# Performance work log

Measured on AMD Instinct MI355X. Metric: run time of the kernel, lower is better.

Reference implementation:

```python
import jax, jax.numpy as jnp
import numpy as np

B, L, T, LM, DFF, D, H = 8, 256, 2048, 4096, 1024, 84, 4
HD = D // H  # 21
NCLS = 265


def _ln(x, s, b):
    m = x.mean(-1, keepdims=True)
    v = ((x - m) ** 2).mean(-1, keepdims=True)
    return (x - m) * jax.lax.rsqrt(v + 1e-5) * s + b


def _fourier(xyz, gB):
    # PositionEmbeddingCoordsSine(d_pos=10, pos_type='fourier'): xyz @ B * 2pi -> [sin, cos]
    proj = (2.0 * jnp.pi) * jnp.einsum('bnc,cd->bnd', xyz, gB)  # [B,N,5]
    return jnp.concatenate([jnp.sin(proj), jnp.cos(proj)], axis=-1)  # [B,N,10]


def setup_inputs() -> dict:
    key = jax.random.key(0)
    ks = jax.random.split(key, 20)
    def nrm(k, shape, scale):
        return jax.random.normal(k, shape, jnp.float32) * scale
    coords = jax.random.uniform(ks[0], (B, L, 6), jnp.float32)
    cls = jax.random.randint(ks[1], (B, L), 0, NCLS).astype(jnp.float32)
    vision_features = jnp.concatenate([coords, cls[..., None]], axis=-1)  # [B,L,7]
    FIN = D * L + LM  # 25600
    inp = {
        'grd_tokens': nrm(ks[2], (T, LM), 1.0),
        'vision_features': vision_features,
        'token_batch_idx': jax.random.randint(ks[3], (T,), 0, B),
        'gauss_B': nrm(ks[4], (3, 5), 1.0),
        'class_emb': nrm(ks[5], (NCLS, 64), 0.02),
        'w_in': nrm(ks[6], (2, D, 3 * D), D ** -0.5),
        'b_in': jnp.zeros((2, 3 * D), jnp.float32),
        'w_out': nrm(ks[7], (2, D, D), D ** -0.5),
        'b_out': jnp.zeros((2, D), jnp.float32),
        'ln1_s': jnp.ones((2, D), jnp.float32), 'ln1_b': jnp.zeros((2, D), jnp.float32),
        'w_ff1': nrm(ks[8], (2, D, DFF), D ** -0.5), 'b_ff1': jnp.zeros((2, DFF), jnp.float32),
        'w_ff2': nrm(ks[9], (2, DFF, D), DFF ** -0.5), 'b_ff2': jnp.zeros((2, D), jnp.float32),
        'ln2_s': jnp.ones((2, D), jnp.float32), 'ln2_b': jnp.zeros((2, D), jnp.float32),
        'w0': nrm(ks[10], (FIN, DFF), FIN ** -0.5), 'b0': jnp.zeros((DFF,), jnp.float32),
        'w1': nrm(ks[11], (DFF, DFF), DFF ** -0.5), 'b1': jnp.zeros((DFF,), jnp.float32),
        'w2': nrm(ks[12], (DFF, DFF), DFF ** -0.5), 'b2': jnp.zeros((DFF,), jnp.float32),
        'w3': nrm(ks[13], (DFF, DFF), DFF ** -0.5), 'b3': jnp.zeros((DFF,), jnp.float32),
        'w4': nrm(ks[14], (DFF, 6), DFF ** -0.5), 'b4': jnp.zeros((6,), jnp.float32),
    }
    return inp


def reference(grd_tokens, vision_features, token_batch_idx, gauss_B, class_emb,
              w_in, b_in, w_out, b_out, ln1_s, ln1_b, w_ff1, b_ff1, w_ff2, b_ff2,
              ln2_s, ln2_b, w0, b0, w1, b1, w2, b2, w3, b3, w4, b4):
    pe_min = _fourier(vision_features[:, :, 0:3], gauss_B)  # [B,L,10]
    pe_max = _fourier(vision_features[:, :, 3:6], gauss_B)  # [B,L,10]
    cls = vision_features[:, :, -1].astype(jnp.int32)
    src = jnp.concatenate([pe_min, pe_max, class_emb[cls]], axis=-1)  # [B,L,84]
    pad = jnp.all(vision_features == 0, axis=-1)  # [B,L]
    neg = jnp.where(pad, -1e9, 0.0)[:, None, None, :]  # [B,1,1,L] key-padding bias
    # 2-layer post-norm transformer encoder (DETR-style, pos=None, dropout=0)
    for l in range(2):
        qkv = src @ w_in[l] + b_in[l]
        q, k, v = jnp.split(qkv, 3, axis=-1)
        q = q.reshape(B, L, H, HD)
        k = k.reshape(B, L, H, HD)
        v = v.reshape(B, L, H, HD)
        scores = jnp.einsum('blhd,bmhd->bhlm', q, k) / jnp.sqrt(jnp.float32(HD)) + neg
        attn = jax.nn.softmax(scores, axis=-1)
        o = jnp.einsum('bhlm,bmhd->blhd', attn, v).reshape(B, L, D)
        src = _ln(src + o @ w_out[l] + b_out[l], ln1_s[l], ln1_b[l])
        ff = jax.nn.relu(src @ w_ff1[l] + b_ff1[l]) @ w_ff2[l] + b_ff2[l]
        src = _ln(src + ff, ln2_s[l], ln2_b[l])
    vision_flat = src.reshape(B, L * D)  # flattened encoder output per sample [B, 21504]
    # batched version of the ragged python loop: gather per-token vision feat + concat lm feat
    feat = jnp.concatenate([vision_flat[token_batch_idx], grd_tokens], axis=-1)  # [T, 25600]
    h = jax.nn.relu(feat @ w0 + b0)
    h = jax.nn.relu(h @ w1 + b1)
    h = jax.nn.relu(h @ w2 + b2)
    h = jax.nn.relu(h @ w3 + b3)
    return h @ w4 + b4  # [T, 6]
```

## Files before the change

### kernel.cpp

```cpp
#include <hip/hip_runtime.h>
#include <hip/hip_bf16.h>

#define B_ 8
#define L_ 256
#define T_ 2048
#define LM_ 4096
#define DFF_ 1024
#define D_ 84
#define H_ 4
#define HD_ 21
#define BL_ (B_*L_)
#define VISF_ (L_*D_)
#define VKS 168
#define VCHUNK (VISF_/VKS)
#define AKS 8
#define AKEYS (L_/AKS)

typedef __attribute__((ext_vector_type(8))) short bf16x8;
typedef __attribute__((ext_vector_type(4))) float f32x4;

typedef const __attribute__((address_space(1))) int* gas_p;
typedef __attribute__((address_space(3))) int* las_p;
__device__ __forceinline__ void gld_lds16(const void* g, void* l) {
    __builtin_amdgcn_global_load_lds((gas_p)g, (las_p)l, 16, 0, 0);
}

__global__ void k_build_src(const float* __restrict__ vf, const float* __restrict__ gB,
                            const float* __restrict__ cemb, float* __restrict__ src,
                            float* __restrict__ neg)
{
    int row = blockIdx.x * blockDim.x + threadIdx.x;
    if (row >= BL_) return;
    float v[7];
    bool allz = true;
    #pragma unroll
    for (int c = 0; c < 7; ++c) { v[c] = vf[row*7 + c]; allz = allz && (v[c] == 0.0f); }
    neg[row] = allz ? -1e9f : 0.0f;
    float* s = src + (size_t)row * D_;
    const float TWO_PI = 6.28318530717958647692f;
    #pragma unroll
    for (int d = 0; d < 5; ++d) {
        float pmin = TWO_PI * (v[0]*gB[d] + v[1]*gB[5+d] + v[2]*gB[10+d]);
        float pmax = TWO_PI * (v[3]*gB[d] + v[4]*gB[5+d] + v[5]*gB[10+d]);
        s[d]      = sinf(pmin);  s[5+d]  = cosf(pmin);
        s[10+d]   = sinf(pmax);  s[15+d] = cosf(pmax);
    }
    int cls = (int)v[6];
    const float4* ce = reinterpret_cast<const float4*>(cemb + (size_t)cls*64);
    float4* so = reinterpret_cast<float4*>(s + 20);
    #pragma unroll
    for (int i = 0; i < 16; ++i) so[i] = ce[i];
}

__global__ __launch_bounds__(256) void k_qkv8(const float* __restrict__ src,
        const float* __restrict__ w_in, const float* __restrict__ b_in,
        float* __restrict__ qkv, int lay)
{
    __shared__ float s8[8][D_];
    int r0 = blockIdx.x * 8, tid = threadIdx.x;
    for (int idx = tid; idx < 8*D_; idx += 256) {
        int r = idx / D_, d = idx - r*D_;
        s8[r][d] = src[(size_t)(r0+r)*D_ + d];
    }
    __syncthreads();
    if (tid < 3*D_) {
        const float* w = w_in + (size_t)lay*D_*3*D_ + tid;
        float acc[8] = {};
        for (int d = 0; d < D_; ++d) {
            float wv = w[(size_t)d*3*D_];
            #pragma unroll
            for (int r = 0; r < 8; ++r) acc[r] = fmaf(s8[r][d], wv, acc[r]);
        }
        float bv = b_in[lay*3*D_ + tid];
        #pragma unroll
        for (int r = 0; r < 8; ++r) qkv[(size_t)(r0+r)*(3*D_) + tid] = acc[r] + bv;
    }
}

__global__ __launch_bounds__(256) void k_attn_part(const float* __restrict__ qkv,
        const float* __restrict__ neg, float* __restrict__ part)
{
    __shared__ float ks_[AKEYS*HD_], vs_[AKEYS*HD_], ns[AKEYS];
    int bh = blockIdx.x;
    int b = bh >> 2, h = bh & 3;
    int sp = blockIdx.y;
    int tid = threadIdx.x;
    int k0 = sp * AKEYS;
    for (int idx = tid; idx < AKEYS*HD_; idx += 256) {
        int l = idx / HD_, d = idx - l*HD_;
        size_t base = ((size_t)(b*L_ + k0 + l))*(3*D_) + h*HD_ + d;
        ks_[idx] = qkv[base + D_];
        vs_[idx] = qkv[base + 2*D_];
    }
    if (tid < AKEYS) ns[tid] = neg[b*L_ + k0 + tid];
    __syncthreads();
    float q[HD_];
    {
        size_t base = ((size_t)(b*L_ + tid))*(3*D_) + h*HD_;
        #pragma unroll
        for (int d = 0; d < HD_; ++d) q[d] = qkv[base + d];
    }
    const float scale = 0.21821789023599239f;
    float m_run = -INFINITY, l_run = 0.0f;
    float o[HD_];
    #pragma unroll
    for (int d = 0; d < HD_; ++d) o[d] = 0.0f;
    for (int m = 0; m < AKEYS; ++m) {
        const float* krow = &ks_[m*HD_];
        float sdot = 0.0f;
        #pragma unroll
        for (int d = 0; d < HD_; ++d) sdot = fmaf(q[d], krow[d], sdot);
        float sc = sdot * scale + ns[m];
        float nm = fmaxf(m_run, sc);
        float c = __expf(m_run - nm);
        float p = __expf(sc - nm);
        l_run = l_run * c + p;
        const float* vrow = &vs_[m*HD_];
        #pragma unroll
        for (int d = 0; d < HD_; ++d) o[d] = fmaf(p, vrow[d], o[d]*c);
        m_run = nm;
    }
    float* po = part + (((size_t)bh*AKS + sp)*L_ + tid)*24;
    #pragma unroll
    for (int d = 0; d < HD_; ++d) po[d] = o[d];
    po[21] = m_run;
    po[22] = l_run;
}

__global__ __launch_bounds__(128) void k_oproj_ln(const float* __restrict__ part,
        const float* __restrict__ w_out, const float* __restrict__ b_out,
        const float* __restrict__ ln_s, const float* __restrict__ ln_b,
        float* __restrict__ src, __hip_bfloat16* __restrict__ srcb, int lay)
{
    __shared__ float os[D_];
    __shared__ float r1[128], r2[128];
    int row = blockIdx.x, tid = threadIdx.x;
    int b = row >> 8, q = row & 255;
    if (tid < D_) {
        int h = tid / 21, d = tid - h*21;
        const float* pb = part + (((size_t)(b*H_ + h)*AKS)*L_ + q)*24;
        float m_tot = -INFINITY;
        #pragma unroll
        for (int sp = 0; sp < AKS; ++sp)
            m_tot = fmaxf(m_tot, pb[(size_t)sp*L_*24 + 21]);
        float l_tot = 0.0f, ov = 0.0f;
        #pragma unroll
        for (int sp = 0; sp < AKS; ++sp) {
            const float* pp = pb + (size_t)sp*L_*24;
            float e = __expf(pp[21] - m_tot);
            l_tot = fmaf(pp[22], e, l_tot);
            ov = fmaf(pp[d], e, ov);
        }
        os[tid] = ov / l_tot;
    }
    __syncthreads();
    float y = 0.0f;
    if (tid < D_) {
        const float* w = w_out + (size_t)lay*D_*D_ + tid;
        float acc = b_out[lay*D_ + tid];
        for (int d = 0; d < D_; ++d) acc = fmaf(os[d], w[(size_t)d*D_], acc);
        y = src[(size_t)row*D_ + tid] + acc;
    }
    r1[tid] = (tid < D_) ? y : 0.0f;
    r2[tid] = (tid < D_) ? y*y : 0.0f;
    __syncthreads();
    for (int s = 64; s > 0; s >>= 1) {
        if (tid < s) { r1[tid] += r1[tid+s]; r2[tid] += r2[tid+s]; }
        __syncthreads();
    }
    float mean = r1[0] * (1.0f/D_);
    float var  = r2[0] * (1.0f/D_) - mean*mean;
    float rstd = rsqrtf(var + 1e-5f);
    float out = 0.0f;
    if (tid < D_) {
        out = (y - mean)*rstd*ln_s[lay*D_+tid] + ln_b[lay*D_+tid];
        src[(size_t)row*D_ + tid] = out;
    }
    srcb[(size_t)row*128 + tid] = (tid < D_) ? __float2bfloat16(out)
                                             : __float2bfloat16(0.0f);
}

__global__ __launch_bounds__(256) void k_ff2_mfma(
        const __hip_bfloat16* __restrict__ hb,
        const __hip_bfloat16* __restrict__ wt,
        float* __restrict__ part)
{
    __shared__ __align__(16) __hip_bfloat16 sA[2][4096];
    __shared__ __align__(16) __hip_bfloat16 sB[2][6144];
    int tid = threadIdx.x;
    int bm = blockIdx.x * 64, sp = blockIdx.y;
    int wave = tid >> 6, lane = tid & 63;
    int wr = wave >> 1, wc = wave & 1;
    int l15 = lane & 15, l4 = lane >> 4;
    f32x4 acc[2][3] = {};

    const int a_m0 = tid & 63;
    const int b_i0 = tid,       b_kb0 = b_i0/96, b_n0 = b_i0%96;
    const int b_i1 = tid + 256, b_kb1 = b_i1/96, b_n1 = b_i1%96;
    const int b_i2 = tid + 512, b_kb2 = b_i2/96, b_n2 = b_i2%96;
    const __hip_bfloat16* Ap0 = hb + (size_t)(bm + a_m0)*1024 + sp*128 + (tid>>6)*8;
    const __hip_bfloat16* Ap1 = Ap0 + 32;
    const __hip_bfloat16* Bp0 = wt + (size_t)b_n0*1024 + sp*128 + b_kb0*8;
    const __hip_bfloat16* Bp1 = wt + (size_t)b_n1*1024 + sp*128 + b_kb1*8;
    const __hip_bfloat16* Bp2 = wt + (size_t)b_n2*1024 + sp*128 + b_kb2*8;

    gld_lds16(Ap0, (char*)&sA[0][0] + tid*16);
    gld_lds16(Ap1, (char*)&sA[0][0] + (tid+256)*16);
    gld_lds16(Bp0, (char*)&sB[0][0] + b_i0*16);
    gld_lds16(Bp1, (char*)&sB[0][0] + b_i1*16);
    gld_lds16(Bp2, (char*)&sB[0][0] + b_i2*16);
    #pragma unroll
    for (int t = 0; t < 2; ++t) {
        __syncthreads();
        if (t == 0) {
            gld_lds16(Ap0 + 64, (char*)&sA[1][0] + tid*16);
            gld_lds16(Ap1 + 64, (char*)&sA[1][0] + (tid+256)*16);
            gld_lds16(Bp0 + 64, (char*)&sB[1][0] + b_i0*16);
            gld_lds16(Bp1 + 64, (char*)&sB[1][0] + b_i1*16);
            gld_lds16(Bp2 + 64, (char*)&sB[1][0] + b_i2*16);
        }
        const __hip_bfloat16* sa = &sA[t][0];
        const __hip_bfloat16* sb = &sB[t][0];
        #pragma unroll
        for (int ks = 0; ks < 2; ++ks) {
            bf16x8 af[2], bfr[3];
            #pragma unroll
            for (int mi = 0; mi < 2; ++mi)
                af[mi] = *reinterpret_cast<const bf16x8*>(
                    &sa[(size_t)((ks*4 + l4)*64 + wr*32 + mi*16 + l15) * 8]);
            #pragma unroll
            for (int ni = 0; ni < 3; ++ni)
                bfr[ni] = *reinterpret_cast<const bf16x8*>(
                    &sb[(size_t)((ks*4 + l4)*96 + wc*48 + ni*16 + l15) * 8]);
            #pragma unroll
            for (int mi = 0; mi < 2; ++mi)
                #pragma unroll
                for (int ni = 0; ni < 3; ++ni)
                    acc[mi][ni] = __builtin_amdgcn_mfma_f32_16x16x32_bf16(
                        af[mi], bfr[ni], acc[mi][ni], 0, 0, 0);
        }
    }
    float* po = part + (size_t)sp*(2048*96);
    #pragma unroll
    for (int mi = 0; mi < 2; ++mi)
        #pragma unroll
        for (int reg = 0; reg < 4; ++reg) {
            int row = bm + wr*32 + mi*16 + l4*4 + reg;
            #pragma unroll
            for (int ni = 0; ni < 3; ++ni) {
                int col = wc*48 + ni*16 + l15;
                po[(size_t)row*96 + col] = acc[mi][ni][reg];
            }
        }
}

__global__ __launch_bounds__(128) void k_ff2ln_red(const float* __restrict__ part,
        const float* __restrict__ b_ff2, const float* __restrict__ ln_s,
        const float* __restrict__ ln_b, float* __restrict__ src, int lay)
{
    __shared__ float r1[128], r2[128];
    int row = blockIdx.x, tid = threadIdx.x;
    float y = 0.0f;
    if (tid < D_) {
        #pragma unroll
        for (int sp = 0; sp < 8; ++sp)
            y += part[(size_t)sp*(2048*96) + (size_t)row*96 + tid];
        y += b_ff2[lay*D_ + tid] + src[(size_t)row*D_ + tid];
    }
    r1[tid] = (tid < D_) ? y : 0.0f;
    r2[tid] = (tid < D_) ? y*y : 0.0f;
    __syncthreads();
    for (int s = 64; s > 0; s >>= 1) {
        if (tid < s) { r1[tid] += r1[tid+s]; r2[tid] += r2[tid+s]; }
        __syncthreads();
    }
    float mean = r1[0] * (1.0f/D_);
    float var  = r2[0] * (1.0f/D_) - mean*mean;
    float rstd = rsqrtf(var + 1e-5f);
    if (tid < D_)
        src[(size_t)row*D_ + tid] = (y - mean)*rstd*ln_s[lay*D_+tid] + ln_b[lay*D_+tid];
}

__global__ __launch_bounds__(256) void k_vis_gemm(const float* __restrict__ src,
        const float* __restrict__ w0, float* __restrict__ partials)
{
    __shared__ float vf[8][VCHUNK];
    __shared__ float red[8][256][4];
    int nt = blockIdx.x, sp = blockIdx.y, tid = threadIdx.x;
    int k0 = sp * VCHUNK;
    for (int idx = tid; idx < 8*VCHUNK; idx += 256) {
        int r = idx >> 7, c = idx & 127;
        vf[r][c] = src[(size_t)r*VISF_ + k0 + c];
    }
    __syncthreads();
    int ng = tid & 31;
    int kh = tid >> 5;
    const float* wp = w0 + (size_t)(k0 + kh*16)*DFF_ + nt*128 + ng*4;
    float acc[8][4] = {};
    #pragma unroll 4
    for (int kk = 0; kk < 16; ++kk) {
        float4 w = *reinterpret_cast<const float4*>(wp + (size_t)kk*DFF_);
        #pragma unroll
        for (int m = 0; m < 8; ++m) {
            float sv = vf[m][kh*16 + kk];
            acc[m][0] = fmaf(sv, w.x, acc[m][0]);
            acc[m][1] = fmaf(sv, w.y, acc[m][1]);
            acc[m][2] = fmaf(sv, w.z, acc[m][2]);
            acc[m][3] = fmaf(sv, w.w, acc[m][3]);
        }
    }
    #pragma unroll
    for (int m = 0; m < 8; ++m)
        *reinterpret_cast<float4*>(&red[m][tid][0]) =
            make_float4(acc[m][0], acc[m][1], acc[m][2], acc[m][3]);
    __syncthreads();
    int m2 = tid >> 5, ng2 = tid & 31;
    float4 s = *reinterpret_cast<const float4*>(&red[m2][ng2][0]);
    #pragma unroll
    for (int j = 1; j < 8; ++j) {
        float4 v = *reinterpret_cast<const float4*>(&red[m2][j*32 + ng2][0]);
        s.x += v.x; s.y += v.y; s.z += v.z; s.w += v.w;
    }
    *reinterpret_cast<float4*>(
        &partials[(size_t)sp*8192 + m2*1024 + nt*128 + ng2*4]) = s;
}

__global__ __launch_bounds__(256) void k_vis_red(const float* __restrict__ partials,
        float* __restrict__ vis)
{
    int o = blockIdx.x*256 + threadIdx.x;
    float s = 0.0f;
    for (int sp = 0; sp < VKS; ++sp) s += partials[(size_t)sp*8192 + o];
    vis[o] = s;
}

struct bh4 { __hip_bfloat16 x, y, z, w; };

__global__ __launch_bounds__(256) void k_f2b(const float* __restrict__ in,
        __hip_bfloat16* __restrict__ out, int n4)
{
    int i = blockIdx.x*256 + threadIdx.x;
    if (i >= n4) return;
    float4 v = reinterpret_cast<const float4*>(in)[i];
    bh4 o = { __float2bfloat16(v.x), __float2bfloat16(v.y),
              __float2bfloat16(v.z), __float2bfloat16(v.w) };
    reinterpret_cast<bh4*>(out)[i] = o;
}

__global__ __launch_bounds__(256) void k_wT(const float* __restrict__ W,
        __hip_bfloat16* __restrict__ WT, int K, int N)
{
    __shared__ float t[32][33];
    int kb = blockIdx.x*32, nb = blockIdx.y*32;
    int tx = threadIdx.x & 31, ty = threadIdx.x >> 5;
    #pragma unroll
    for (int i = 0; i < 4; ++i)
        t[ty + i*8][tx] = W[(size_t)(kb + ty + i*8)*N + nb + tx];
    __syncthreads();
    #pragma unroll
    for (int i = 0; i < 4; ++i)
        WT[(size_t)(nb + ty + i*8)*K + kb + tx] = __float2bfloat16(t[tx][ty + i*8]);
}

__global__ __launch_bounds__(256) void k_wTp(const float* __restrict__ W,
        __hip_bfloat16* __restrict__ WT, int K, int N, int KP)
{
    __shared__ float t[32][33];
    int kb = blockIdx.x*32, nb = blockIdx.y*32;
    int tx = threadIdx.x & 31, ty = threadIdx.x >> 5;
    #pragma unroll
    for (int i = 0; i < 4; ++i) {
        int k = kb + ty + i*8, n = nb + tx;
        t[ty + i*8][tx] = (k < K && n < N) ? W[(size_t)k*N + n] : 0.0f;
    }
    __syncthreads();
    #pragma unroll
    for (int i = 0; i < 4; ++i)
        WT[(size_t)(nb + ty + i*8)*KP + kb + tx] = __float2bfloat16(t[tx][ty + i*8]);
}

template<bool ADD_VIS>
__global__ __launch_bounds__(256) void mfma_gemm(
        const __hip_bfloat16* __restrict__ A,
        const __hip_bfloat16* __restrict__ WT,
        const float* __restrict__ bias,
        const float* __restrict__ vis,
        const int* __restrict__ bidx,
        __hip_bfloat16* __restrict__ C,
        int K)
{
    constexpr int N = 1024;
    __shared__ __align__(16) __hip_bfloat16 sA[2][8192];
    __shared__ __align__(16) __hip_bfloat16 sB[2][8192];
    int tid = threadIdx.x;
    int bm = blockIdx.x * 64, bn = blockIdx.y * 64;
    int wave = tid >> 6, lane = tid & 63;
    int wr = wave >> 1, wc = wave & 1;
    int l15 = lane & 15, l4 = lane >> 4;
    f32x4 acc[2][2] = {};

    const __hip_bfloat16* Ap = A  + (size_t)(bm + (tid & 63))*K + (tid >> 6)*8;
    const __hip_bfloat16* Bp = WT + (size_t)(bn + (tid & 63))*K + (tid >> 6)*8;

    int nsteps = K >> 7;
    auto STAGE = [&](int t, int b) {
        int ko = t << 7;
        char* la = (char*)&sA[b][0];
        char* lb = (char*)&sB[b][0];
        #pragma unroll
        for (int r = 0; r < 4; ++r) {
            gld_lds16(Ap + ko + r*32, la + (tid + r*256)*16);
            gld_lds16(Bp + ko + r*32, lb + (tid + r*256)*16);
        }
    };
    STAGE(0, 0);
    for (int t = 0; t < nsteps; ++t) {
        if (t + 1 < nsteps) {
            STAGE(t + 1, (t + 1) & 1);
            asm volatile("s_waitcnt vmcnt(8)" ::: "memory");
        } else {
            asm volatile("s_waitcnt vmcnt(0)" ::: "memory");
        }
        __builtin_amdgcn_s_barrier();
        const __hip_bfloat16* sa = &sA[t & 1][0];
        const __hip_bfloat16* sb = &sB[t & 1][0];
        #pragma unroll
        for (int ks = 0; ks < 4; ++ks) {
            bf16x8 af[2], bfr[2];
            #pragma unroll
            for (int mi = 0; mi < 2; ++mi)
                af[mi] = *reinterpret_cast<const bf16x8*>(
                    &sa[(size_t)((ks*4 + l4)*64 + wr*32 + mi*16 + l15) * 8]);
            #pragma unroll
            for (int ni = 0; ni < 2; ++ni)
                bfr[ni] = *reinterpret_cast<const bf16x8*>(
                    &sb[(size_t)((ks*4 + l4)*64 + wc*32 + ni*16 + l15) * 8]);
            #pragma unroll
            for (int mi = 0; mi < 2; ++mi)
                #pragma unroll
                for (int ni = 0; ni < 2; ++ni)
                    acc[mi][ni] = __builtin_amdgcn_mfma_f32_16x16x32_bf16(
                        af[mi], bfr[ni], acc[mi][ni], 0, 0, 0);
        }
        __builtin_amdgcn_s_barrier();
    }

    #pragma unroll
    for (int mi = 0; mi < 2; ++mi) {
        #pragma unroll
        for (int reg = 0; reg < 4; ++reg) {
            int row = bm + wr*32 + mi*16 + l4*4 + reg;
            const float* vrow = nullptr;
            if (ADD_VIS) vrow = vis + (size_t)bidx[row]*1024;
            #pragma unroll
            for (int ni = 0; ni < 2; ++ni) {
                int col = bn + wc*32 + ni*16 + l15;
                float v = acc[mi][ni][reg] + bias[col];
                if (ADD_VIS) v += vrow[col];
                v = fmaxf(v, 0.0f);
                C[(size_t)row*N + col] = __float2bfloat16(v);
            }
        }
    }
}

__global__ __launch_bounds__(64) void k_final(const __hip_bfloat16* __restrict__ h,
        const float* __restrict__ w4, const float* __restrict__ b4, float* __restrict__ out)
{
    int t = blockIdx.x, lane = threadIdx.x;
    float acc[6] = {};
    for (int k = lane; k < DFF_; k += 64) {
        float hv = __bfloat162float(h[(size_t)t*DFF_ + k]);
        #pragma unroll
        for (int j = 0; j < 6; ++j) acc[j] = fmaf(hv, w4[k*6 + j], acc[j]);
    }
    #pragma unroll
    for (int j = 0; j < 6; ++j)
        #pragma unroll
        for (int s = 32; s > 0; s >>= 1) acc[j] += __shfl_down(acc[j], s);
    if (lane == 0) {
        #pragma unroll
        for (int j = 0; j < 6; ++j) out[(size_t)t*6 + j] = acc[j] + b4[j];
    }
}

extern "C" void kernel_launch(void* const* d_in, const int* in_sizes, int n_in,
                              void* d_out, int out_size, void* d_ws, size_t ws_size,
                              hipStream_t stream)
{
    const float* grd   = (const float*)d_in[0];
    const float* vfeat = (const float*)d_in[1];
    const int*   tbi   = (const int*)  d_in[2];
    const float* gB    = (const float*)d_in[3];
    const float* cemb  = (const float*)d_in[4];
    const float* w_in  = (const float*)d_in[5];
    const float* b_in  = (const float*)d_in[6];
    const float* w_out = (const float*)d_in[7];
    const float* b_out = (const float*)d_in[8];
    const float* ln1_s = (const float*)d_in[9];
    const float* ln1_b = (const float*)d_in[10];
    const float* w_ff1 = (const float*)d_in[11];
    const float* b_ff1 = (const float*)d_in[12];
    const float* w_ff2 = (const float*)d_in[13];
    const float* b_ff2 = (const float*)d_in[14];
    const float* ln2_s = (const float*)d_in[15];
    const float* ln2_b = (const float*)d_in[16];
    const float* w0    = (const float*)d_in[17];
    const float* b0    = (const float*)d_in[18];
    const float* w1    = (const float*)d_in[19];
    const float* b1    = (const float*)d_in[20];
    const float* w2    = (const float*)d_in[21];
    const float* b2    = (const float*)d_in[22];
    const float* w3    = (const float*)d_in[23];
    const float* b3    = (const float*)d_in[24];
    const float* w4    = (const float*)d_in[25];
    const float* b4    = (const float*)d_in[26];

    float* ws = (float*)d_ws;
    float* src    = ws;
    float* neg    = src    + 172032;
    float* qkv    = neg    + 2048;
    float* attn_o = qkv    + 516096;
    float* vparts = attn_o + 172032;
    float* vp2    = vparts + 1376256;
    float* visp   = vp2    + 98304;
    float* ffpart = visp   + 8192;
    float* fend   = ffpart + 1572864;
    __hip_bfloat16* grdb  = (__hip_bfloat16*)fend;
    __hip_bfloat16* w0t   = grdb  + 8388608;
    __hip_bfloat16* w1t   = w0t   + 4194304;
    __hip_bfloat16* w2t   = w1t   + 1048576;
    __hip_bfloat16* w3t   = w2t   + 1048576;
    __hip_bfloat16* hab   = w3t   + 1048576;
    __hip_bfloat16* hbb   = hab   + 2097152;
    __hip_bfloat16* srcb  = hbb   + 2097152;
    __hip_bfloat16* wff1t = srcb  + 262144;
    __hip_bfloat16* wff2t = wff1t + 262144;
    __hip_bfloat16* ffh   = hab;

    k_f2b<<<(T_*LM_/4 + 255)/256, 256, 0, stream>>>(grd, grdb, T_*LM_/4);
    k_wT<<<dim3(LM_/32,  DFF_/32), 256, 0, stream>>>(w0 + (size_t)VISF_*DFF_, w0t, LM_,  DFF_);
    k_wT<<<dim3(DFF_/32, DFF_/32), 256, 0, stream>>>(w1, w1t, DFF_, DFF_);
    k_wT<<<dim3(DFF_/32, DFF_/32), 256, 0, stream>>>(w2, w2t, DFF_, DFF_);
    k_wT<<<dim3(DFF_/32, DFF_/32), 256, 0, stream>>>(w3, w3t, DFF_, DFF_);
    for (int l = 0; l < 2; ++l) {
        k_wTp<<<dim3(128/32, 1024/32), 256, 0, stream>>>(
            w_ff1 + (size_t)l*D_*DFF_, wff1t + (size_t)l*1024*128, D_, DFF_, 128);
        k_wTp<<<dim3(1024/32, 96/32),  256, 0, stream>>>(
            w_ff2 + (size_t)l*DFF_*D_, wff2t + (size_t)l*96*1024, DFF_, D_, 1024);
    }

    k_build_src<<<8, 256, 0, stream>>>(vfeat, gB, cemb, src, neg);

    for (int lay = 0; lay < 2; ++lay) {
        k_qkv8      <<<BL_/8, 256, 0, stream>>>(src, w_in, b_in, qkv, lay);
        k_attn_part <<<dim3(B_*H_, AKS), 256, 0, stream>>>(qkv, neg, ffpart);
        k_oproj_ln  <<<BL_, 128, 0, stream>>>(ffpart, w_out, b_out, ln1_s, ln1_b, src, srcb, lay);
        mfma_gemm<false><<<dim3(32, 16), 256, 0, stream>>>(
            srcb, wff1t + (size_t)lay*1024*128, b_ff1 + lay*DFF_,
            nullptr, nullptr, ffh, 128);
        k_ff2_mfma<<<dim3(32, 8), 256, 0, stream>>>(
            ffh, wff2t + (size_t)lay*96*1024, ffpart);
        k_ff2ln_red<<<BL_, 128, 0, stream>>>(ffpart, b_ff2, ln2_s, ln2_b, src, lay);
    }

    k_vis_gemm<<<dim3(8, VKS), 256, 0, stream>>>(src, w0, vparts);
    k_vis_red<<<32, 256, 0, stream>>>(vparts, visp);

    dim3 mg(T_/64, DFF_/64);
    mfma_gemm<true ><<<mg, 256, 0, stream>>>(grdb, w0t, b0, visp, tbi, hab, LM_);
    mfma_gemm<false><<<mg, 256, 0, stream>>>(hab,  w1t, b1, nullptr, nullptr, hbb, DFF_);
    mfma_gemm<false><<<mg, 256, 0, stream>>>(hbb,  w2t, b2, nullptr, nullptr, hab, DFF_);
    mfma_gemm<false><<<mg, 256, 0, stream>>>(hab,  w3t, b3, nullptr, nullptr, hbb, DFF_);

    k_final<<<T_, 64, 0, stream>>>(hbb, w4, b4, (float*)d_out);
}
```

Baseline: 294.6 us.

## Pack GEMM operands into MFMA-fragment tiled layout and drop LDS staging

Activations and weights are now stored in a 16-row by 8-k blocked layout that matches the MFMA fragment, so each lane loads its fragment directly from global memory with 16-byte loads. The GEMM no longer stages through LDS with double buffering, and it uses a wider 64x128 tile with the output written back packed via LDS. Every producer and consumer (layernorm output, ff2, the final head, the weight transposes) is changed to the packed layout. This removes LDS traffic and barriers, but global loads are no longer overlapped by an explicit prefetch pipeline.

```diff
diff --git a/kernel.cpp b/kernel.cpp
--- a/kernel.cpp
+++ b/kernel.cpp
@@ -25,6 +25,9 @@
     __builtin_amdgcn_global_load_lds((gas_p)g, (las_p)l, 16, 0, 0);
 }
 
+struct bh4 { __hip_bfloat16 x, y, z, w; };
+
+
 __global__ void k_build_src(const float* __restrict__ vf, const float* __restrict__ gB,
                             const float* __restrict__ cemb, float* __restrict__ src,
                             float* __restrict__ neg)
@@ -176,8 +179,8 @@
         out = (y - mean)*rstd*ln_s[lay*D_+tid] + ln_b[lay*D_+tid];
         src[(size_t)row*D_ + tid] = out;
     }
-    srcb[(size_t)row*128 + tid] = (tid < D_) ? __float2bfloat16(out)
-                                             : __float2bfloat16(0.0f);
+    __hip_bfloat16 val = (tid < D_) ? __float2bfloat16(out) : __float2bfloat16(0.0f);
+    srcb[((size_t)(row>>4)*16 + (tid>>3))*128 + (row&15)*8 + (tid&7)] = val;
 }
 
 __global__ __launch_bounds__(256) void k_ff2_mfma(
@@ -194,12 +197,13 @@
     int l15 = lane & 15, l4 = lane >> 4;
     f32x4 acc[2][3] = {};
 
-    const int a_m0 = tid & 63;
+    const int row0 = bm + (tid & 63);
+    const int kb = tid >> 6;
+    const __hip_bfloat16* Ap0 = hb + (((size_t)(row0 >> 4)*128) + sp*16 + kb)*128 + (row0 & 15)*8;
+    const __hip_bfloat16* Ap1 = Ap0 + 512;
     const int b_i0 = tid,       b_kb0 = b_i0/96, b_n0 = b_i0%96;
     const int b_i1 = tid + 256, b_kb1 = b_i1/96, b_n1 = b_i1%96;
     const int b_i2 = tid + 512, b_kb2 = b_i2/96, b_n2 = b_i2%96;
-    const __hip_bfloat16* Ap0 = hb + (size_t)(bm + a_m0)*1024 + sp*128 + (tid>>6)*8;
-    const __hip_bfloat16* Ap1 = Ap0 + 32;
     const __hip_bfloat16* Bp0 = wt + (size_t)b_n0*1024 + sp*128 + b_kb0*8;
     const __hip_bfloat16* Bp1 = wt + (size_t)b_n1*1024 + sp*128 + b_kb1*8;
     const __hip_bfloat16* Bp2 = wt + (size_t)b_n2*1024 + sp*128 + b_kb2*8;
@@ -213,8 +217,8 @@
     for (int t = 0; t < 2; ++t) {
         __syncthreads();
         if (t == 0) {
-            gld_lds16(Ap0 + 64, (char*)&sA[1][0] + tid*16);
-            gld_lds16(Ap1 + 64, (char*)&sA[1][0] + (tid+256)*16);
+            gld_lds16(Ap0 + 1024, (char*)&sA[1][0] + tid*16);
+            gld_lds16(Ap1 + 1024, (char*)&sA[1][0] + (tid+256)*16);
             gld_lds16(Bp0 + 64, (char*)&sB[1][0] + b_i0*16);
             gld_lds16(Bp1 + 64, (char*)&sB[1][0] + b_i1*16);
             gld_lds16(Bp2 + 64, (char*)&sB[1][0] + b_i2*16);
@@ -334,21 +338,24 @@
     vis[o] = s;
 }
 
-struct bh4 { __hip_bfloat16 x, y, z, w; };
-
-__global__ __launch_bounds__(256) void k_f2b(const float* __restrict__ in,
-        __hip_bfloat16* __restrict__ out, int n4)
+__global__ __launch_bounds__(256) void k_f2b_pack(const float* __restrict__ in,
+        __hip_bfloat16* __restrict__ out)
 {
     int i = blockIdx.x*256 + threadIdx.x;
-    if (i >= n4) return;
-    float4 v = reinterpret_cast<const float4*>(in)[i];
-    bh4 o = { __float2bfloat16(v.x), __float2bfloat16(v.y),
-              __float2bfloat16(v.z), __float2bfloat16(v.w) };
-    reinterpret_cast<bh4*>(out)[i] = o;
-}
-
-__global__ __launch_bounds__(256) void k_wT(const float* __restrict__ W,
-        __hip_bfloat16* __restrict__ WT, int K, int N)
+    int row = i >> 9, kc = i & 511;
+    const float4* p = reinterpret_cast<const float4*>(in + (size_t)row*4096 + kc*8);
+    float4 v0 = p[0], v1 = p[1];
+    bh4 a = { __float2bfloat16(v0.x), __float2bfloat16(v0.y),
+              __float2bfloat16(v0.z), __float2bfloat16(v0.w) };
+    bh4 b = { __float2bfloat16(v1.x), __float2bfloat16(v1.y),
+              __float2bfloat16(v1.z), __float2bfloat16(v1.w) };
+    __hip_bfloat16* o = out + ((size_t)(row>>4)*512 + kc)*128 + (row&15)*8;
+    reinterpret_cast<bh4*>(o)[0] = a;
+    reinterpret_cast<bh4*>(o)[1] = b;
+}
+
+__global__ __launch_bounds__(256) void k_wT_pack(const float* __restrict__ W,
+        __hip_bfloat16* __restrict__ Wp, int K, int N)
 {
     __shared__ float t[32][33];
     int kb = blockIdx.x*32, nb = blockIdx.y*32;
@@ -357,13 +364,16 @@
     for (int i = 0; i < 4; ++i)
         t[ty + i*8][tx] = W[(size_t)(kb + ty + i*8)*N + nb + tx];
     __syncthreads();
-    #pragma unroll
-    for (int i = 0; i < 4; ++i)
-        WT[(size_t)(nb + ty + i*8)*K + kb + tx] = __float2bfloat16(t[tx][ty + i*8]);
-}
-
-__global__ __launch_bounds__(256) void k_wTp(const float* __restrict__ W,
-        __hip_bfloat16* __restrict__ WT, int K, int N, int KP)
+    int KG = K >> 3;
+    #pragma unroll
+    for (int i = 0; i < 4; ++i) {
+        int n = nb + ty + i*8, k = kb + tx;
+        Wp[((size_t)(n>>4)*KG + (k>>3))*128 + (n&15)*8 + (k&7)] = __float2bfloat16(t[tx][ty + i*8]);
+    }
+}
+
+__global__ __launch_bounds__(256) void k_wTp_pack(const float* __restrict__ W,
+        __hip_bfloat16* __restrict__ Wp, int K, int N, int KP)
 {
     __shared__ float t[32][33];
     int kb = blockIdx.x*32, nb = blockIdx.y*32;
@@ -374,105 +384,116 @@
         t[ty + i*8][tx] = (k < K && n < N) ? W[(size_t)k*N + n] : 0.0f;
     }
     __syncthreads();
+    int KG = KP >> 3;
+    #pragma unroll
+    for (int i = 0; i < 4; ++i) {
+        int n = nb + ty + i*8, k = kb + tx;
+        Wp[((size_t)(n>>4)*KG + (k>>3))*128 + (n&15)*8 + (k&7)] = __float2bfloat16(t[tx][ty + i*8]);
+    }
+}
+
+__global__ __launch_bounds__(256) void k_wTp(const float* __restrict__ W,
+        __hip_bfloat16* __restrict__ WT, int K, int N, int KP)
+{
+    __shared__ float t[32][33];
+    int kb = blockIdx.x*32, nb = blockIdx.y*32;
+    int tx = threadIdx.x & 31, ty = threadIdx.x >> 5;
+    #pragma unroll
+    for (int i = 0; i < 4; ++i) {
+        int k = kb + ty + i*8, n = nb + tx;
+        t[ty + i*8][tx] = (k < K && n < N) ? W[(size_t)k*N + n] : 0.0f;
+    }
+    __syncthreads();
     #pragma unroll
     for (int i = 0; i < 4; ++i)
         WT[(size_t)(nb + ty + i*8)*KP + kb + tx] = __float2bfloat16(t[tx][ty + i*8]);
 }
 
-template<bool ADD_VIS>
+template<bool ADD_VIS, int K>
 __global__ __launch_bounds__(256) void mfma_gemm(
-        const __hip_bfloat16* __restrict__ A,
-        const __hip_bfloat16* __restrict__ WT,
+        const __hip_bfloat16* __restrict__ Ap,
+        const __hip_bfloat16* __restrict__ Bp,
         const float* __restrict__ bias,
         const float* __restrict__ vis,
         const int* __restrict__ bidx,
-        __hip_bfloat16* __restrict__ C,
-        int K)
-{
-    constexpr int N = 1024;
-    __shared__ __align__(16) __hip_bfloat16 sA[2][8192];
-    __shared__ __align__(16) __hip_bfloat16 sB[2][8192];
-    int tid = threadIdx.x;
-    int bm = blockIdx.x * 64, bn = blockIdx.y * 64;
-    int wave = tid >> 6, lane = tid & 63;
+        __hip_bfloat16* __restrict__ Cp)
+{
+    constexpr int KG = K >> 3;
+    constexpr int NG = 128;
+    __shared__ __align__(16) __hip_bfloat16 cst[64*128];
+    int tid = threadIdx.x, wave = tid >> 6, lane = tid & 63;
     int wr = wave >> 1, wc = wave & 1;
     int l15 = lane & 15, l4 = lane >> 4;
-    f32x4 acc[2][2] = {};
-
-    const __hip_bfloat16* Ap = A  + (size_t)(bm + (tid & 63))*K + (tid >> 6)*8;
-    const __hip_bfloat16* Bp = WT + (size_t)(bn + (tid & 63))*K + (tid >> 6)*8;
-
-    int nsteps = K >> 7;
-    auto STAGE = [&](int t, int b) {
-        int ko = t << 7;
-        char* la = (char*)&sA[b][0];
-        char* lb = (char*)&sB[b][0];
-        #pragma unroll
-        for (int r = 0; r < 4; ++r) {
-            gld_lds16(Ap + ko + r*32, la + (tid + r*256)*16);
-            gld_lds16(Bp + ko + r*32, lb + (tid + r*256)*16);
-        }
-    };
-    STAGE(0, 0);
-    for (int t = 0; t < nsteps; ++t) {
-        if (t + 1 < nsteps) {
-            STAGE(t + 1, (t + 1) & 1);
-            asm volatile("s_waitcnt vmcnt(8)" ::: "memory");
-        } else {
-            asm volatile("s_waitcnt vmcnt(0)" ::: "memory");
-        }
-        __builtin_amdgcn_s_barrier();
-        const __hip_bfloat16* sa = &sA[t & 1][0];
-        const __hip_bfloat16* sb = &sB[t & 1][0];
-        #pragma unroll
-        for (int ks = 0; ks < 4; ++ks) {
-            bf16x8 af[2], bfr[2];
-            #pragma unroll
-            for (int mi = 0; mi < 2; ++mi)
-                af[mi] = *reinterpret_cast<const bf16x8*>(
-                    &sa[(size_t)((ks*4 + l4)*64 + wr*32 + mi*16 + l15) * 8]);
-            #pragma unroll
-            for (int ni = 0; ni < 2; ++ni)
-                bfr[ni] = *reinterpret_cast<const bf16x8*>(
-                    &sb[(size_t)((ks*4 + l4)*64 + wc*32 + ni*16 + l15) * 8]);
-            #pragma unroll
-            for (int mi = 0; mi < 2; ++mi)
-                #pragma unroll
-                for (int ni = 0; ni < 2; ++ni)
-                    acc[mi][ni] = __builtin_amdgcn_mfma_f32_16x16x32_bf16(
-                        af[mi], bfr[ni], acc[mi][ni], 0, 0, 0);
-        }
-        __builtin_amdgcn_s_barrier();
+    int bm = blockIdx.x * 64, bn = blockIdx.y * 128;
+    const __hip_bfloat16* Aw = Ap + ((size_t)((bm >> 4) + wr*2) * KG) * 128 + lane*8;
+    const __hip_bfloat16* Bw = Bp + ((size_t)((bn >> 4) + wc*4) * KG) * 128 + lane*8;
+    f32x4 acc[2][4] = {};
+
+    #pragma unroll 4
+    for (int kg = 0; kg < KG; kg += 4) {
+        bf16x8 a[2], b[4];
+        #pragma unroll
+        for (int mi = 0; mi < 2; ++mi)
+            a[mi] = *reinterpret_cast<const bf16x8*>(Aw + ((size_t)mi*KG + kg)*128);
+        #pragma unroll
+        for (int ni = 0; ni < 4; ++ni)
+            b[ni] = *reinterpret_cast<const bf16x8*>(Bw + ((size_t)ni*KG + kg)*128);
+        #pragma unroll
+        for (int mi = 0; mi < 2; ++mi)
+            #pragma unroll
+            for (int ni = 0; ni < 4; ++ni)
+                acc[mi][ni] = __builtin_amdgcn_mfma_f32_16x16x32_bf16(
+                    a[mi], b[ni], acc[mi][ni], 0, 0, 0);
     }
 
     #pragma unroll
     for (int mi = 0; mi < 2; ++mi) {
-        #pragma unroll
-        for (int reg = 0; reg < 4; ++reg) {
-            int row = bm + wr*32 + mi*16 + l4*4 + reg;
-            const float* vrow = nullptr;
-            if (ADD_VIS) vrow = vis + (size_t)bidx[row]*1024;
-            #pragma unroll
-            for (int ni = 0; ni < 2; ++ni) {
-                int col = bn + wc*32 + ni*16 + l15;
-                float v = acc[mi][ni][reg] + bias[col];
-                if (ADD_VIS) v += vrow[col];
+        int mg = wr*2 + mi;
+        #pragma unroll
+        for (int ni = 0; ni < 4; ++ni) {
+            int cg = wc*8 + ni*2 + (l15 >> 3);
+            int c  = l15 & 7;
+            int col = bn + cg*8 + c;
+            float bv = bias[col];
+            #pragma unroll
+            for (int reg = 0; reg < 4; ++reg) {
+                int r = l4*4 + reg;
+                float v = acc[mi][ni][reg] + bv;
+                if (ADD_VIS) v += vis[(size_t)bidx[bm + mg*16 + r]*1024 + col];
                 v = fmaxf(v, 0.0f);
-                C[(size_t)row*N + col] = __float2bfloat16(v);
+                cst[((mg*16 + cg)*16 + r)*8 + c] = __float2bfloat16(v);
             }
         }
     }
-}
-
-__global__ __launch_bounds__(64) void k_final(const __hip_bfloat16* __restrict__ h,
+    __syncthreads();
+    #pragma unroll
+    for (int ch = tid; ch < 1024; ch += 256) {
+        int mgcg = ch >> 4, r = ch & 15;
+        int mg = mgcg >> 4, cg = mgcg & 15;
+        size_t go = ((size_t)((bm >> 4) + mg) * NG + (bn >> 3) + cg) * 128 + r*8;
+        *reinterpret_cast<bf16x8*>(Cp + go) =
+            *reinterpret_cast<const bf16x8*>(cst + (size_t)ch*8);
+    }
+}
+
+__global__ __launch_bounds__(64) void k_final(const __hip_bfloat16* __restrict__ hp,
         const float* __restrict__ w4, const float* __restrict__ b4, float* __restrict__ out)
 {
     int t = blockIdx.x, lane = threadIdx.x;
+    int mg = t >> 4, r = t & 15;
     float acc[6] = {};
-    for (int k = lane; k < DFF_; k += 64) {
-        float hv = __bfloat162float(h[(size_t)t*DFF_ + k]);
-        #pragma unroll
-        for (int j = 0; j < 6; ++j) acc[j] = fmaf(hv, w4[k*6 + j], acc[j]);
+    #pragma unroll
+    for (int it = 0; it < 2; ++it) {
+        int kg = lane + it*64;
+        bf16x8 h = *reinterpret_cast<const bf16x8*>(hp + ((size_t)mg*128 + kg)*128 + r*8);
+        #pragma unroll
+        for (int j = 0; j < 8; ++j) {
+            unsigned short us = (unsigned short)h[j];
+            float hv = __uint_as_float((unsigned)us << 16);
+            int k = kg*8 + j;
+            #pragma unroll
+            for (int c = 0; c < 6; ++c) acc[c] = fmaf(hv, w4[k*6 + c], acc[c]);
+        }
     }
     #pragma unroll
     for (int j = 0; j < 6; ++j)
@@ -520,10 +541,8 @@
     float* src    = ws;
     float* neg    = src    + 172032;
     float* qkv    = neg    + 2048;
-    float* attn_o = qkv    + 516096;
-    float* vparts = attn_o + 172032;
-    float* vp2    = vparts + 1376256;
-    float* visp   = vp2    + 98304;
+    float* vparts = qkv    + 516096;
+    float* visp   = vparts + 1376256;
     float* ffpart = visp   + 8192;
     float* fend   = ffpart + 1572864;
     __hip_bfloat16* grdb  = (__hip_bfloat16*)fend;
@@ -538,27 +557,26 @@
     __hip_bfloat16* wff2t = wff1t + 262144;
     __hip_bfloat16* ffh   = hab;
 
-    k_f2b<<<(T_*LM_/4 + 255)/256, 256, 0, stream>>>(grd, grdb, T_*LM_/4);
-    k_wT<<<dim3(LM_/32,  DFF_/32), 256, 0, stream>>>(w0 + (size_t)VISF_*DFF_, w0t, LM_,  DFF_);
-    k_wT<<<dim3(DFF_/32, DFF_/32), 256, 0, stream>>>(w1, w1t, DFF_, DFF_);
-    k_wT<<<dim3(DFF_/32, DFF_/32), 256, 0, stream>>>(w2, w2t, DFF_, DFF_);
-    k_wT<<<dim3(DFF_/32, DFF_/32), 256, 0, stream>>>(w3, w3t, DFF_, DFF_);
+    k_f2b_pack<<<4096, 256, 0, stream>>>(grd, grdb);
+    k_wT_pack<<<dim3(LM_/32,  DFF_/32), 256, 0, stream>>>(w0 + (size_t)VISF_*DFF_, w0t, LM_,  DFF_);
+    k_wT_pack<<<dim3(DFF_/32, DFF_/32), 256, 0, stream>>>(w1, w1t, DFF_, DFF_);
+    k_wT_pack<<<dim3(DFF_/32, DFF_/32), 256, 0, stream>>>(w2, w2t, DFF_, DFF_);
+    k_wT_pack<<<dim3(DFF_/32, DFF_/32), 256, 0, stream>>>(w3, w3t, DFF_, DFF_);
     for (int l = 0; l < 2; ++l) {
-        k_wTp<<<dim3(128/32, 1024/32), 256, 0, stream>>>(
+        k_wTp_pack<<<dim3(128/32, 1024/32), 256, 0, stream>>>(
             w_ff1 + (size_t)l*D_*DFF_, wff1t + (size_t)l*1024*128, D_, DFF_, 128);
-        k_wTp<<<dim3(1024/32, 96/32),  256, 0, stream>>>(
+        k_wTp<<<dim3(1024/32, 96/32), 256, 0, stream>>>(
             w_ff2 + (size_t)l*DFF_*D_, wff2t + (size_t)l*96*1024, DFF_, D_, 1024);
     }
 
     k_build_src<<<8, 256, 0, stream>>>(vfeat, gB, cemb, src, neg);
 
     for (int lay = 0; lay < 2; ++lay) {
-        k_qkv8      <<<BL_/8, 256, 0, stream>>>(src, w_in, b_in, qkv, lay);
-        k_attn_part <<<dim3(B_*H_, AKS), 256, 0, stream>>>(qkv, neg, ffpart);
-        k_oproj_ln  <<<BL_, 128, 0, stream>>>(ffpart, w_out, b_out, ln1_s, ln1_b, src, srcb, lay);
-        mfma_gemm<false><<<dim3(32, 16), 256, 0, stream>>>(
-            srcb, wff1t + (size_t)lay*1024*128, b_ff1 + lay*DFF_,
-            nullptr, nullptr, ffh, 128);
+        k_qkv8     <<<BL_/8, 256, 0, stream>>>(src, w_in, b_in, qkv, lay);
+        k_attn_part<<<dim3(B_*H_, AKS), 256, 0, stream>>>(qkv, neg, ffpart);
+        k_oproj_ln <<<BL_, 128, 0, stream>>>(ffpart, w_out, b_out, ln1_s, ln1_b, src, srcb, lay);
+        mfma_gemm<false, 128><<<dim3(32, 8), 256, 0, stream>>>(
+            srcb, wff1t + (size_t)lay*1024*128, b_ff1 + lay*DFF_, nullptr, nullptr, ffh);
         k_ff2_mfma<<<dim3(32, 8), 256, 0, stream>>>(
             ffh, wff2t + (size_t)lay*96*1024, ffpart);
         k_ff2ln_red<<<BL_, 128, 0, stream>>>(ffpart, b_ff2, ln2_s, ln2_b, src, lay);
@@ -567,11 +585,11 @@
     k_vis_gemm<<<dim3(8, VKS), 256, 0, stream>>>(src, w0, vparts);
     k_vis_red<<<32, 256, 0, stream>>>(vparts, visp);
 
-    dim3 mg(T_/64, DFF_/64);
-    mfma_gemm<true ><<<mg, 256, 0, stream>>>(grdb, w0t, b0, visp, tbi, hab, LM_);
-    mfma_gemm<false><<<mg, 256, 0, stream>>>(hab,  w1t, b1, nullptr, nullptr, hbb, DFF_);
-    mfma_gemm<false><<<mg, 256, 0, stream>>>(hbb,  w2t, b2, nullptr, nullptr, hab, DFF_);
-    mfma_gemm<false><<<mg, 256, 0, stream>>>(hab,  w3t, b3, nullptr, nullptr, hbb, DFF_);
+    dim3 mg(T_/64, DFF_/128);
+    mfma_gemm<true,  LM_ ><<<mg, 256, 0, stream>>>(grdb, w0t, b0, visp, tbi, hab);
+    mfma_gemm<false, DFF_><<<mg, 256, 0, stream>>>(hab,  w1t, b1, nullptr, nullptr, hbb);
+    mfma_gemm<false, DFF_><<<mg, 256, 0, stream>>>(hbb,  w2t, b2, nullptr, nullptr, hab);
+    mfma_gemm<false, DFF_><<<mg, 256, 0, stream>>>(hab,  w3t, b3, nullptr, nullptr, hbb);
 
     k_final<<<T_, 64, 0, stream>>>(hbb, w4, b4, (float*)d_out);
 }
```

Measured after the change: 261.1 us. -11.4%, faster.
